# Performance work log

Measured on AMD Instinct MI355X. Metric: run time of the kernel, lower is better.

Reference implementation:

```python
import jax, jax.numpy as jnp
import numpy as np

# Model config (matches init_kwargs)
B, N, D = 4, 4096, 1024
H, DH = 16, 64            # heads, dim_head (H*DH == D)
SEG, RATIO = 64, 2        # LongNet segment length and dilation ratio
DFF = 4 * D
EPS = 1e-5


def layer_norm(x, g, b):
    m = jnp.mean(x, axis=-1, keepdims=True)
    v = jnp.var(x, axis=-1, keepdims=True)
    return (x - m) * jax.lax.rsqrt(v + EPS) * g + b


def dilated_attention(x, wq, bq, wk, bk, wv, bv, wo, bo):
    # LongNet-style dilated attention: split into segments of SEG tokens,
    # each head attends over every RATIO-th token of its segment, with the
    # dilation offset distributed across heads (offset = head % RATIO).
    b, n, d = x.shape
    G = n // SEG          # number of segments
    M = SEG // RATIO      # dilated segment length
    scale = DH ** -0.5

    def proj_split(w, bias):
        t = (x @ w + bias).reshape(b, G, SEG, H, DH)
        return t.transpose(0, 1, 3, 2, 4)  # [B, G, H, SEG, DH]

    q = proj_split(wq, bq)
    k = proj_split(wk, bk)
    v = proj_split(wv, bv)

    # per-head dilated indices within a segment: [H, M]
    idx = (jnp.arange(H)[:, None] % RATIO) + RATIO * jnp.arange(M)[None, :]
    gidx = idx[None, None, :, :, None]  # broadcast to [1,1,H,M,1]
    qs = jnp.take_along_axis(q, gidx, axis=3)  # [B,G,H,M,DH]
    ks = jnp.take_along_axis(k, gidx, axis=3)
    vs = jnp.take_along_axis(v, gidx, axis=3)

    scores = jnp.einsum('bghmd,bghnd->bghmn', qs, ks) * scale
    p = jax.nn.softmax(scores, axis=-1)
    o = jnp.einsum('bghmn,bghnd->bghmd', p, vs)  # [B,G,H,M,DH]

    # scatter dilated outputs back to full segment positions (zeros elsewhere)
    full = jnp.zeros((b, G, H, SEG, DH), dtype=o.dtype)
    full = full.at[:, :, jnp.arange(H)[:, None], idx, :].set(o)
    out = full.transpose(0, 1, 3, 2, 4).reshape(b, n, d)
    return out @ wo + bo


def setup_inputs() -> dict:
    key = jax.random.key(0)
    ks = jax.random.split(key, 8)
    sd = D ** -0.5
    inp = {
        'x': jax.random.normal(ks[0], (B, N, D), jnp.float32),
        'gamma': jnp.ones((D,), jnp.float32),  # shared pre-norm (beta is zero buffer)
        'wq': jax.random.normal(ks[1], (D, D), jnp.float32) * sd,
        'bq': jnp.zeros((D,), jnp.float32),
        'wk': jax.random.normal(ks[2], (D, D), jnp.float32) * sd,
        'bk': jnp.zeros((D,), jnp.float32),
        'wv': jax.random.normal(ks[3], (D, D), jnp.float32) * sd,
        'bv': jnp.zeros((D,), jnp.float32),
        'wo': jax.random.normal(ks[4], (D, D), jnp.float32) * sd,
        'bo': jnp.zeros((D,), jnp.float32),
        'ff_g': jnp.ones((D,), jnp.float32),   # FFN LayerNorm weight
        'ff_b': jnp.zeros((D,), jnp.float32),  # FFN LayerNorm bias
        'w1': jax.random.normal(ks[5], (D, DFF), jnp.float32) * sd,
        'b1': jnp.zeros((DFF,), jnp.float32),
        'w2': jax.random.normal(ks[6], (DFF, D), jnp.float32) * (DFF ** -0.5),
        'b2': jnp.zeros((D,), jnp.float32),
    }
    return inp


def reference(x, gamma, wq, bq, wk, bk, wv, bv, wo, bo, ff_g, ff_b, w1, b1, w2, b2):
    zero = jnp.zeros((D,), x.dtype)
    # attention sub-block (pre-norm, residual)
    h = layer_norm(x, gamma, zero)
    attn = dilated_attention(h, wq, bq, wk, bk, wv, bv, wo, bo)
    x = x + attn
    # FFN sub-block (outer shared norm, then FFN's own LayerNorm per FeedForward)
    h = layer_norm(x, gamma, zero)
    h = layer_norm(h, ff_g, ff_b)
    h = jax.nn.gelu(h @ w1 + b1, approximate=False) @ w2 + b2
    return x + h
```

## Files before the change

### kernel.cpp

```cpp
#include <hip/hip_runtime.h>
#include <hip/hip_bf16.h>
#include <math.h>

#define NTOK 16384
#define DM   1024
#define NQKV 3072
#define DFF  4096

typedef __bf16 bf16;
typedef __bf16 bf16x8 __attribute__((ext_vector_type(8)));
typedef float  f32x4  __attribute__((ext_vector_type(4)));

__device__ __forceinline__ void gload_lds16(const bf16* g, bf16* l) {
  __builtin_amdgcn_global_load_lds((const __attribute__((address_space(1))) void*)g,
                                   (__attribute__((address_space(3))) void*)l,
                                   16, 0, 0);
}

#define BAR()    asm volatile("s_barrier" ::: "memory")
#define SB0()    __builtin_amdgcn_sched_barrier(0)
#define LGKM(N)  asm volatile("s_waitcnt lgkmcnt(" #N ")" ::: "memory")
#define VMW4()   asm volatile("s_waitcnt vmcnt(4)" ::: "memory")
#define VMW0()   asm volatile("s_waitcnt vmcnt(0)" ::: "memory")

__global__ __launch_bounds__(256)
void transpose_cvt(const float* __restrict__ src, bf16* __restrict__ dst, int K, int N)
{
  __shared__ float t[32][33];
  const int tx = threadIdx.x & 31, ty = threadIdx.x >> 5;
  const int n0 = blockIdx.x * 32, k0 = blockIdx.y * 32;
#pragma unroll
  for (int i = 0; i < 4; ++i)
    t[ty + 8*i][tx] = src[(size_t)(k0 + ty + 8*i) * N + n0 + tx];
  __syncthreads();
#pragma unroll
  for (int i = 0; i < 4; ++i)
    dst[(size_t)(n0 + ty + 8*i) * K + k0 + tx] = (bf16)t[tx][ty + 8*i];
}

__global__ void concat_bias(const float* __restrict__ bq, const float* __restrict__ bk,
                            const float* __restrict__ bv, float* __restrict__ o)
{
  int i = blockIdx.x * 256 + threadIdx.x;
  o[i] = (i < 1024) ? bq[i] : (i < 2048 ? bk[i - 1024] : bv[i - 2048]);
}

__global__ __launch_bounds__(256)
void ln1_kernel(const float* __restrict__ x, const float* __restrict__ gamma,
                bf16* __restrict__ out)
{
  __shared__ float2 red[4];
  const int row = blockIdx.x, tid = threadIdx.x;
  const float4 v = ((const float4*)(x + (size_t)row * DM))[tid];
  float s  = v.x + v.y + v.z + v.w;
  float s2 = v.x*v.x + v.y*v.y + v.z*v.z + v.w*v.w;
#pragma unroll
  for (int m = 32; m >= 1; m >>= 1) { s += __shfl_xor(s, m); s2 += __shfl_xor(s2, m); }
  if ((tid & 63) == 0) red[tid >> 6] = make_float2(s, s2);
  __syncthreads();
  float S  = red[0].x + red[1].x + red[2].x + red[3].x;
  float S2 = red[0].y + red[1].y + red[2].y + red[3].y;
  const float mean = S * (1.0f / DM);
  const float var  = S2 * (1.0f / DM) - mean * mean;
  const float rs   = rsqrtf(var + 1e-5f);
  const float4 g = ((const float4*)gamma)[tid];
  union { bf16 b[4]; uint2 u; } o;
  o.b[0] = (bf16)((v.x - mean) * rs * g.x);
  o.b[1] = (bf16)((v.y - mean) * rs * g.y);
  o.b[2] = (bf16)((v.z - mean) * rs * g.z);
  o.b[3] = (bf16)((v.w - mean) * rs * g.w);
  *(uint2*)(out + (size_t)row * DM + tid * 4) = o.u;
}

__global__ __launch_bounds__(256)
void ln2_kernel(const float* __restrict__ x, const float* __restrict__ gamma,
                const float* __restrict__ ffg, const float* __restrict__ ffb,
                bf16* __restrict__ out)
{
  __shared__ float2 red[4];
  const int row = blockIdx.x, tid = threadIdx.x;
  const float4 v = ((const float4*)(x + (size_t)row * DM))[tid];
  float s  = v.x + v.y + v.z + v.w;
  float s2 = v.x*v.x + v.y*v.y + v.z*v.z + v.w*v.w;
#pragma unroll
  for (int m = 32; m >= 1; m >>= 1) { s += __shfl_xor(s, m); s2 += __shfl_xor(s2, m); }
  if ((tid & 63) == 0) red[tid >> 6] = make_float2(s, s2);
  __syncthreads();
  float S  = red[0].x + red[1].x + red[2].x + red[3].x;
  float S2 = red[0].y + red[1].y + red[2].y + red[3].y;
  float mean = S * (1.0f / DM);
  float var  = S2 * (1.0f / DM) - mean * mean;
  float rs   = rsqrtf(var + 1e-5f);
  const float4 g = ((const float4*)gamma)[tid];
  float y0 = (v.x - mean) * rs * g.x;
  float y1 = (v.y - mean) * rs * g.y;
  float y2 = (v.z - mean) * rs * g.z;
  float y3 = (v.w - mean) * rs * g.w;
  __syncthreads();
  s  = y0 + y1 + y2 + y3;
  s2 = y0*y0 + y1*y1 + y2*y2 + y3*y3;
#pragma unroll
  for (int m = 32; m >= 1; m >>= 1) { s += __shfl_xor(s, m); s2 += __shfl_xor(s2, m); }
  if ((tid & 63) == 0) red[tid >> 6] = make_float2(s, s2);
  __syncthreads();
  S  = red[0].x + red[1].x + red[2].x + red[3].x;
  S2 = red[0].y + red[1].y + red[2].y + red[3].y;
  mean = S * (1.0f / DM);
  var  = S2 * (1.0f / DM) - mean * mean;
  rs   = rsqrtf(var + 1e-5f);
  const float4 a = ((const float4*)ffg)[tid];
  const float4 bb = ((const float4*)ffb)[tid];
  union { bf16 b[4]; uint2 u; } o;
  o.b[0] = (bf16)((y0 - mean) * rs * a.x + bb.x);
  o.b[1] = (bf16)((y1 - mean) * rs * a.y + bb.y);
  o.b[2] = (bf16)((y2 - mean) * rs * a.z + bb.z);
  o.b[3] = (bf16)((y3 - mean) * rs * a.w + bb.w);
  *(uint2*)(out + (size_t)row * DM + tid * 4) = o.u;
}


#define A_OFF(buf, mh) (((buf)*2 + (mh)) * 8192)
#define B_OFF(buf, nh) (32768 + ((buf)*2 + (nh)) * 8192)

__device__ __forceinline__ void mmaq(f32x4 (&acc)[8][4], bf16x8 (&a)[4][2],
                                     bf16x8 (&b)[2][2], int mh, int nh)
{
  __builtin_amdgcn_s_setprio(1);
#pragma unroll
  for (int i = 0; i < 4; ++i)
#pragma unroll
    for (int j = 0; j < 2; ++j)
#pragma unroll
      for (int kk = 0; kk < 2; ++kk)
        acc[mh*4 + i][nh*2 + j] =
          __builtin_amdgcn_mfma_f32_16x16x32_bf16(a[i][kk], b[j][kk],
                                                  acc[mh*4 + i][nh*2 + j], 0, 0, 0);
  __builtin_amdgcn_s_setprio(0);
}

template<int EPI>
__global__ __launch_bounds__(512, 2)
void gemm256(const bf16* __restrict__ A, int lda,
             const bf16* __restrict__ Bt,
             const float* __restrict__ bias,
             const float* res, int ldres,
             void* Cout, int ldc, int K, int nblk)
{
  __shared__ __align__(16) bf16 lds[65536];
  const int tid = threadIdx.x, lane = tid & 63, wave = tid >> 6;
  const int wm = wave >> 2, wn = wave & 3;
  const int l16 = lane & 15, lg = lane >> 4;

  int id = blockIdx.x;
  id = (id & 7) * (nblk >> 3) + (id >> 3);
  const int row0 = (id & 63) << 8;
  const int col0 = (id >> 6) << 8;
  const int NT = K >> 6;

  const char* Ab = (const char*)A;
  const char* Bb = (const char*)Bt;
  unsigned oA[2][2], oB[2][2];
  {
    const int lr = lane >> 3, lc = lane & 7;
#pragma unroll
    for (int l = 0; l < 2; ++l) {
      const int rho = (wave * 2 + l) * 8 + lr;
      const int gc = ((lc ^ (rho & 7)) << 3);
#pragma unroll
      for (int hf = 0; hf < 2; ++hf) {
        const int ga = (rho >> 6) * 128 + hf * 64 + (rho & 63);
        const int gb = (rho >> 5) * 64 + hf * 32 + (rho & 31);
        oA[hf][l] = (unsigned)(((row0 + ga) * lda + gc) * 2);
        oB[hf][l] = (unsigned)(((col0 + gb) * K + gc) * 2);
      }
    }
  }
  const int so = wave * 1024 + lane * 8;

#define STAGE_A(hf, OFF) do { \
    gload_lds16((const bf16*)(Ab + oA[hf][0]), (bf16*)lds + (OFF) + so); \
    gload_lds16((const bf16*)(Ab + oA[hf][1]), (bf16*)lds + (OFF) + so + 512); \
    oA[hf][0] += 128; oA[hf][1] += 128; } while (0)
#define STAGE_B(hf, OFF) do { \
    gload_lds16((const bf16*)(Bb + oB[hf][0]), (bf16*)lds + (OFF) + so); \
    gload_lds16((const bf16*)(Bb + oB[hf][1]), (bf16*)lds + (OFF) + so + 512); \
    oB[hf][0] += 128; oB[hf][1] += 128; } while (0)

  int aoff[4][2], boff[2][2];
#pragma unroll
  for (int i = 0; i < 4; ++i) {
    const int rho = wm * 64 + i * 16 + l16;
#pragma unroll
    for (int kk = 0; kk < 2; ++kk)
      aoff[i][kk] = rho * 64 + (((kk * 4 + lg) ^ (rho & 7)) << 3);
  }
#pragma unroll
  for (int j = 0; j < 2; ++j) {
    const int rho = wn * 32 + j * 16 + l16;
#pragma unroll
    for (int kk = 0; kk < 2; ++kk)
      boff[j][kk] = rho * 64 + (((kk * 4 + lg) ^ (rho & 7)) << 3);
  }

#define LDAF(OFF) do { \
    af[0][0] = *(const bf16x8*)&lds[(OFF) + aoff[0][0]]; \
    af[0][1] = *(const bf16x8*)&lds[(OFF) + aoff[0][1]]; \
    af[1][0] = *(const bf16x8*)&lds[(OFF) + aoff[1][0]]; \
    af[1][1] = *(const bf16x8*)&lds[(OFF) + aoff[1][1]]; \
    af[2][0] = *(const bf16x8*)&lds[(OFF) + aoff[2][0]]; \
    af[2][1] = *(const bf16x8*)&lds[(OFF) + aoff[2][1]]; \
    af[3][0] = *(const bf16x8*)&lds[(OFF) + aoff[3][0]]; \
    af[3][1] = *(const bf16x8*)&lds[(OFF) + aoff[3][1]]; } while (0)
#define LDBF(dst, OFF) do { \
    dst[0][0] = *(const bf16x8*)&lds[(OFF) + boff[0][0]]; \
    dst[0][1] = *(const bf16x8*)&lds[(OFF) + boff[0][1]]; \
    dst[1][0] = *(const bf16x8*)&lds[(OFF) + boff[1][0]]; \
    dst[1][1] = *(const bf16x8*)&lds[(OFF) + boff[1][1]]; } while (0)

  f32x4 acc[8][4] = {};
  bf16x8 af[4][2], b0f[2][2], b1f[2][2];

  STAGE_A(0, A_OFF(0, 0)); STAGE_B(0, B_OFF(0, 0));
  STAGE_A(1, A_OFF(0, 1)); STAGE_B(1, B_OFF(0, 1));
  if (NT > 1) { STAGE_A(0, A_OFF(1, 0)); STAGE_B(0, B_OFF(1, 0)); VMW4(); }
  else        { VMW0(); }
  BAR();

#define TILE_BODY(BUF) do { \
    const bool p1 = (t + 1) < NT, p2 = (t + 2) < NT; \
    LDAF(A_OFF(BUF, 0)); \
    LDBF(b0f, B_OFF(BUF, 0)); \
    LDBF(b1f, B_OFF(BUF, 1)); \
    if (p1) STAGE_A(1, A_OFF(BUF ^ 1, 1)); \
    LGKM(4); SB0(); \
    mmaq(acc, af, b0f, 0, 0); \
    BAR(); \
    if (p1) STAGE_B(1, B_OFF(BUF ^ 1, 1)); \
    LGKM(0); SB0(); \
    mmaq(acc, af, b1f, 0, 1); \
    LDAF(A_OFF(BUF, 1)); \
    BAR(); \
    if (p2) STAGE_A(0, A_OFF(BUF, 0)); \
    LGKM(0); SB0(); \
    mmaq(acc, af, b0f, 1, 0); \
    BAR(); \
    if (p2) STAGE_B(0, B_OFF(BUF, 0)); \
    mmaq(acc, af, b1f, 1, 1); \
    if (p2) { VMW4(); } else { VMW0(); } \
    BAR(); } while (0)

  for (int t = 0; t < NT; ++t) {
    TILE_BODY(0);
    ++t;
    TILE_BODY(1);
  }

#pragma unroll
  for (int i = 0; i < 8; ++i) {
    const int m0 = row0 + wm * 128 + (i >> 2) * 64 + (i & 3) * 16 + lg * 4;
#pragma unroll
    for (int j = 0; j < 4; ++j) {
      const int n = col0 + wn * 64 + (j >> 1) * 32 + (j & 1) * 16 + l16;
      const float bv = bias[n];
#pragma unroll
      for (int r = 0; r < 4; ++r) {
        const long m = m0 + r;
        float v = acc[i][j][r] + bv;
        if constexpr (EPI == 0) {
          ((bf16*)Cout)[m * ldc + n] = (bf16)v;
        } else if constexpr (EPI == 1) {
          ((float*)Cout)[m * ldc + n] = v + res[m * ldres + n];
        } else {
          float gl = 0.5f * v * (1.0f + erff(v * 0.70710678118654752f));
          ((bf16*)Cout)[m * ldc + n] = (bf16)gl;
        }
      }
    }
  }
}

__global__ __launch_bounds__(64)
void attn_kernel(bf16* qkv)
{
  __shared__ bf16 Plds[32 * 32];
  __shared__ bf16 vT[64 * 32];
  const int blk = blockIdx.x;
  const int h = blk & 15;
  const int g = (blk >> 4) & 63;
  const int b = blk >> 10;
  const int par = h & 1;
  const int lane = threadIdx.x;
  const int l16 = lane & 15, lg = lane >> 4;
  const long base = ((long)b * 4096 + g * 64) * NQKV;

  bf16x8 qf[2][2], kf[2][2];
#pragma unroll
  for (int mb = 0; mb < 2; ++mb) {
    const int s = par + 2 * (mb * 16 + l16);
    const bf16* qrow = qkv + base + (long)s * NQKV + h * 64;
#pragma unroll
    for (int kk = 0; kk < 2; ++kk) {
      qf[mb][kk] = *(const bf16x8*)(qrow + kk * 32 + lg * 8);
      kf[mb][kk] = *(const bf16x8*)(qrow + 1024 + kk * 32 + lg * 8);
    }
  }

#pragma unroll
  for (int it = 0; it < 4; ++it) {
    const int kr  = it * 8 + (lane >> 3);
    const int dh0 = (lane & 7) * 8;
    const int s = par + 2 * kr;
    union { uint4 u; bf16 e[8]; } vv;
    vv.u = *(const uint4*)(qkv + base + (long)s * NQKV + 2048 + h * 64 + dh0);
#pragma unroll
    for (int j = 0; j < 8; ++j)
      vT[(dh0 + j) * 32 + kr] = vv.e[j];
  }

  f32x4 sc[2][2] = {};
#pragma unroll
  for (int mb = 0; mb < 2; ++mb)
#pragma unroll
    for (int nb = 0; nb < 2; ++nb)
#pragma unroll
      for (int kk = 0; kk < 2; ++kk)
        sc[mb][nb] = __builtin_amdgcn_mfma_f32_16x16x32_bf16(qf[mb][kk], kf[nb][kk], sc[mb][nb], 0, 0, 0);

  float pr[2][2][4];
#pragma unroll
  for (int mb = 0; mb < 2; ++mb)
#pragma unroll
    for (int r = 0; r < 4; ++r) {
      float a0 = sc[mb][0][r] * 0.125f, a1 = sc[mb][1][r] * 0.125f;
      float mx = fmaxf(a0, a1);
#pragma unroll
      for (int msk = 8; msk >= 1; msk >>= 1) mx = fmaxf(mx, __shfl_xor(mx, msk));
      float e0 = expf(a0 - mx), e1 = expf(a1 - mx);
      float sm = e0 + e1;
#pragma unroll
      for (int msk = 8; msk >= 1; msk >>= 1) sm += __shfl_xor(sm, msk);
      float inv = 1.0f / sm;
      pr[mb][0][r] = e0 * inv;
      pr[mb][1][r] = e1 * inv;
    }

  __syncthreads();
#pragma unroll
  for (int mb = 0; mb < 2; ++mb)
#pragma unroll
    for (int nb = 0; nb < 2; ++nb)
#pragma unroll
      for (int r = 0; r < 4; ++r)
        Plds[(mb * 16 + lg * 4 + r) * 32 + nb * 16 + l16] = (bf16)pr[mb][nb][r];
  __syncthreads();

  bf16x8 pa[2], vb[4];
#pragma unroll
  for (int mb = 0; mb < 2; ++mb)
    pa[mb] = *(const bf16x8*)&Plds[(mb * 16 + l16) * 32 + lg * 8];
#pragma unroll
  for (int nb = 0; nb < 4; ++nb)
    vb[nb] = *(const bf16x8*)&vT[(nb * 16 + l16) * 32 + lg * 8];
  f32x4 oc[2][4] = {};
#pragma unroll
  for (int mb = 0; mb < 2; ++mb)
#pragma unroll
    for (int nb = 0; nb < 4; ++nb)
      oc[mb][nb] = __builtin_amdgcn_mfma_f32_16x16x32_bf16(pa[mb], vb[nb], oc[mb][nb], 0, 0, 0);

#pragma unroll
  for (int mb = 0; mb < 2; ++mb)
#pragma unroll
    for (int nb = 0; nb < 4; ++nb)
#pragma unroll
      for (int r = 0; r < 4; ++r) {
        const int m = mb * 16 + lg * 4 + r;
        const int s = par + 2 * m;
        qkv[base + (long)s * NQKV + h * 64 + nb * 16 + l16] = (bf16)oc[mb][nb][r];
      }
  const uint4 z = make_uint4(0, 0, 0, 0);
#pragma unroll
  for (int it = 0; it < 4; ++it) {
    const int r2 = it * 8 + (lane >> 3);
    const int s = (1 - par) + 2 * r2;
    *(uint4*)(qkv + base + (long)s * NQKV + h * 64 + (lane & 7) * 8) = z;
  }
}

extern "C" void kernel_launch(void* const* d_in, const int* in_sizes, int n_in,
                              void* d_out, int out_size, void* d_ws, size_t ws_size,
                              hipStream_t stream)
{
  const float* x     = (const float*)d_in[0];
  const float* gamma = (const float*)d_in[1];
  const float* wq = (const float*)d_in[2];  const float* bq = (const float*)d_in[3];
  const float* wk = (const float*)d_in[4];  const float* bk = (const float*)d_in[5];
  const float* wv = (const float*)d_in[6];  const float* bv = (const float*)d_in[7];
  const float* wo = (const float*)d_in[8];  const float* bo = (const float*)d_in[9];
  const float* ffg = (const float*)d_in[10]; const float* ffb = (const float*)d_in[11];
  const float* w1 = (const float*)d_in[12]; const float* b1 = (const float*)d_in[13];
  const float* w2 = (const float*)d_in[14]; const float* b2 = (const float*)d_in[15];

  char* p = (char*)d_ws;
  bf16* Wqkv_t = (bf16*)p; p += (size_t)NQKV * DM * 2;
  bf16* Wo_t   = (bf16*)p; p += (size_t)DM * DM * 2;
  bf16* W1_t   = (bf16*)p; p += (size_t)DFF * DM * 2;
  bf16* W2_t   = (bf16*)p; p += (size_t)DM * DFF * 2;
  float* bqkv  = (float*)p; p += (size_t)NQKV * 4;
  bf16* hbuf   = (bf16*)p; p += (size_t)NTOK * DM * 2;
  bf16* qkv    = (bf16*)p; p += (size_t)NTOK * DFF * 2;
  float* xnew  = (float*)d_out;

  dim3 b256(256);
  transpose_cvt<<<dim3(32, 32),  b256, 0, stream>>>(wq, Wqkv_t,               DM, DM);
  transpose_cvt<<<dim3(32, 32),  b256, 0, stream>>>(wk, Wqkv_t + 1024 * 1024, DM, DM);
  transpose_cvt<<<dim3(32, 32),  b256, 0, stream>>>(wv, Wqkv_t + 2048 * 1024, DM, DM);
  transpose_cvt<<<dim3(32, 32),  b256, 0, stream>>>(wo, Wo_t, DM, DM);
  transpose_cvt<<<dim3(128, 32), b256, 0, stream>>>(w1, W1_t, DM, DFF);
  transpose_cvt<<<dim3(32, 128), b256, 0, stream>>>(w2, W2_t, DFF, DM);
  concat_bias<<<12, b256, 0, stream>>>(bq, bk, bv, bqkv);

  ln1_kernel<<<NTOK, b256, 0, stream>>>(x, gamma, hbuf);

  gemm256<0><<<dim3(768), 512, 0, stream>>>(
      hbuf, DM, Wqkv_t, bqkv, nullptr, 0, qkv, NQKV, DM, 768);

  attn_kernel<<<4096, dim3(64), 0, stream>>>(qkv);

  gemm256<1><<<dim3(256), 512, 0, stream>>>(
      qkv, NQKV, Wo_t, bo, x, DM, xnew, DM, DM, 256);

  ln2_kernel<<<NTOK, b256, 0, stream>>>(xnew, gamma, ffg, ffb, hbuf);

  gemm256<2><<<dim3(1024), 512, 0, stream>>>(
      hbuf, DM, W1_t, b1, nullptr, 0, qkv, DFF, DM, 1024);

  gemm256<1><<<dim3(256), 512, 0, stream>>>(
      qkv, DFF, W2_t, b2, xnew, DM, (float*)d_out, DM, DFF, 256);
}
```

Baseline: 683.8 us.

## Deepen GEMM main-loop prefetch with double-buffered A fragments and peeled tail

Restructures the GEMM K-loop so both full tiles are staged before the loop starts, and LDS-to-register fragment loads for the next half-tile are issued before the current MFMA group runs. A and B fragments are double-buffered in registers and the last two tiles are peeled into a drain sequence. The aim is to hide LDS and global-load latency behind MFMAs with fewer stalls per barrier, at the cost of more VGPRs and an assumption that NT is even and at least 2.

```diff
diff --git a/kernel.cpp b/kernel.cpp
--- a/kernel.cpp
+++ b/kernel.cpp
@@ -20,8 +20,7 @@
 #define BAR()    asm volatile("s_barrier" ::: "memory")
 #define SB0()    __builtin_amdgcn_sched_barrier(0)
 #define LGKM(N)  asm volatile("s_waitcnt lgkmcnt(" #N ")" ::: "memory")
-#define VMW4()   asm volatile("s_waitcnt vmcnt(4)" ::: "memory")
-#define VMW0()   asm volatile("s_waitcnt vmcnt(0)" ::: "memory")
+#define VMW(N)   asm volatile("s_waitcnt vmcnt(" #N ")" ::: "memory")
 
 __global__ __launch_bounds__(256)
 void transpose_cvt(const float* __restrict__ src, bf16* __restrict__ dst, int K, int N)
@@ -202,15 +201,15 @@
       boff[j][kk] = rho * 64 + (((kk * 4 + lg) ^ (rho & 7)) << 3);
   }
 
-#define LDAF(OFF) do { \
-    af[0][0] = *(const bf16x8*)&lds[(OFF) + aoff[0][0]]; \
-    af[0][1] = *(const bf16x8*)&lds[(OFF) + aoff[0][1]]; \
-    af[1][0] = *(const bf16x8*)&lds[(OFF) + aoff[1][0]]; \
-    af[1][1] = *(const bf16x8*)&lds[(OFF) + aoff[1][1]]; \
-    af[2][0] = *(const bf16x8*)&lds[(OFF) + aoff[2][0]]; \
-    af[2][1] = *(const bf16x8*)&lds[(OFF) + aoff[2][1]]; \
-    af[3][0] = *(const bf16x8*)&lds[(OFF) + aoff[3][0]]; \
-    af[3][1] = *(const bf16x8*)&lds[(OFF) + aoff[3][1]]; } while (0)
+#define LDAF(dst, OFF) do { \
+    dst[0][0] = *(const bf16x8*)&lds[(OFF) + aoff[0][0]]; \
+    dst[0][1] = *(const bf16x8*)&lds[(OFF) + aoff[0][1]]; \
+    dst[1][0] = *(const bf16x8*)&lds[(OFF) + aoff[1][0]]; \
+    dst[1][1] = *(const bf16x8*)&lds[(OFF) + aoff[1][1]]; \
+    dst[2][0] = *(const bf16x8*)&lds[(OFF) + aoff[2][0]]; \
+    dst[2][1] = *(const bf16x8*)&lds[(OFF) + aoff[2][1]]; \
+    dst[3][0] = *(const bf16x8*)&lds[(OFF) + aoff[3][0]]; \
+    dst[3][1] = *(const bf16x8*)&lds[(OFF) + aoff[3][1]]; } while (0)
 #define LDBF(dst, OFF) do { \
     dst[0][0] = *(const bf16x8*)&lds[(OFF) + boff[0][0]]; \
     dst[0][1] = *(const bf16x8*)&lds[(OFF) + boff[0][1]]; \
@@ -218,42 +217,60 @@
     dst[1][1] = *(const bf16x8*)&lds[(OFF) + boff[1][1]]; } while (0)
 
   f32x4 acc[8][4] = {};
-  bf16x8 af[4][2], b0f[2][2], b1f[2][2];
+  bf16x8 af0[4][2], af1[4][2], b0[2][2], b1[2][2];
 
   STAGE_A(0, A_OFF(0, 0)); STAGE_B(0, B_OFF(0, 0));
   STAGE_A(1, A_OFF(0, 1)); STAGE_B(1, B_OFF(0, 1));
-  if (NT > 1) { STAGE_A(0, A_OFF(1, 0)); STAGE_B(0, B_OFF(1, 0)); VMW4(); }
-  else        { VMW0(); }
+  STAGE_A(0, A_OFF(1, 0)); STAGE_B(0, B_OFF(1, 0));
+  STAGE_A(1, A_OFF(1, 1)); STAGE_B(1, B_OFF(1, 1));
+  VMW(8);
   BAR();
-
-#define TILE_BODY(BUF) do { \
-    const bool p1 = (t + 1) < NT, p2 = (t + 2) < NT; \
-    LDAF(A_OFF(BUF, 0)); \
-    LDBF(b0f, B_OFF(BUF, 0)); \
-    LDBF(b1f, B_OFF(BUF, 1)); \
-    if (p1) STAGE_A(1, A_OFF(BUF ^ 1, 1)); \
-    LGKM(4); SB0(); \
-    mmaq(acc, af, b0f, 0, 0); \
+  LDAF(af0, A_OFF(0, 0));
+  LDBF(b0,  B_OFF(0, 0));
+
+#define FULL(BUF) do { \
+    LDBF(b1, B_OFF(BUF, 1)); \
+    LGKM(4); \
+    STAGE_A(0, A_OFF(BUF, 0)); \
+    SB0(); mmaq(acc, af0, b0, 0, 0); \
     BAR(); \
-    if (p1) STAGE_B(1, B_OFF(BUF ^ 1, 1)); \
-    LGKM(0); SB0(); \
-    mmaq(acc, af, b1f, 0, 1); \
-    LDAF(A_OFF(BUF, 1)); \
+    LDAF(af1, A_OFF(BUF, 1)); \
+    LGKM(8); \
+    STAGE_B(0, B_OFF(BUF, 0)); \
+    SB0(); mmaq(acc, af0, b1, 0, 1); \
+    VMW(8); \
     BAR(); \
-    if (p2) STAGE_A(0, A_OFF(BUF, 0)); \
-    LGKM(0); SB0(); \
-    mmaq(acc, af, b0f, 1, 0); \
+    LDAF(af0, A_OFF((BUF) ^ 1, 0)); \
+    LGKM(8); \
+    STAGE_A(1, A_OFF(BUF, 1)); \
+    SB0(); mmaq(acc, af1, b0, 1, 0); \
     BAR(); \
-    if (p2) STAGE_B(0, B_OFF(BUF, 0)); \
-    mmaq(acc, af, b1f, 1, 1); \
-    if (p2) { VMW4(); } else { VMW0(); } \
+    LDBF(b0, B_OFF((BUF) ^ 1, 0)); \
+    STAGE_B(1, B_OFF(BUF, 1)); \
+    SB0(); mmaq(acc, af1, b1, 1, 1); \
+    VMW(8); \
     BAR(); } while (0)
 
-  for (int t = 0; t < NT; ++t) {
-    TILE_BODY(0);
-    ++t;
-    TILE_BODY(1);
-  }
+  for (int t = 0; t < NT - 2; t += 2) {
+    FULL(0);
+    FULL(1);
+  }
+
+  LDBF(b1, B_OFF(0, 1));
+  LGKM(4); SB0(); mmaq(acc, af0, b0, 0, 0); BAR();
+  LDAF(af1, A_OFF(0, 1));
+  LGKM(8); SB0(); mmaq(acc, af0, b1, 0, 1); VMW(4); BAR();
+  LDAF(af0, A_OFF(1, 0));
+  LGKM(8); SB0(); mmaq(acc, af1, b0, 1, 0); BAR();
+  LDBF(b0, B_OFF(1, 0));
+  SB0(); mmaq(acc, af1, b1, 1, 1); VMW(0); BAR();
+
+  LDBF(b1, B_OFF(1, 1));
+  LGKM(4); SB0(); mmaq(acc, af0, b0, 0, 0); BAR();
+  LDAF(af1, A_OFF(1, 1));
+  LGKM(8); SB0(); mmaq(acc, af0, b1, 0, 1); BAR();
+  LGKM(0); SB0(); mmaq(acc, af1, b0, 1, 0); BAR();
+  SB0(); mmaq(acc, af1, b1, 1, 1);
 
 #pragma unroll
   for (int i = 0; i < 8; ++i) {
```

Result: slower. 1.010 ms (+47.6%).
